# Kernel optimization log

Measured on AMD Instinct MI355X. Metric: run time of the kernel, lower is better.

Reference implementation:

```python
import jax, jax.numpy as jnp
import numpy as np

B, S, H, DH = 8, 2048, 16, 64
D = H * DH  # 1024; also the input feature dim
BIG_NEG = 1e8


def setup_inputs() -> dict:
    key = jax.random.key(0)
    ks = jax.random.split(key, 7)
    glorot = lambda k, shp: jax.random.normal(k, shp, jnp.float32) * np.sqrt(2.0 / (shp[0] + shp[1]))
    return {
        "Q_seq": jax.random.normal(ks[0], (B, S, D), jnp.float32),
        "K_seq": jax.random.normal(ks[1], (B, S, D), jnp.float32),
        "Q_mask": jnp.ones((B, S), jnp.float32),
        "K_mask": jnp.ones((B, S), jnp.float32),
        "WQ": glorot(ks[2], (D, D)),
        "WK": glorot(ks[3], (D, D)),
        "Wq": glorot(ks[4], (D, H)),
        "Wk": glorot(ks[5], (D, H)),
        "WP": glorot(ks[6], (D, D)),
    }


def reference(Q_seq, B_K_seq=None, **_unused):
    raise NotImplementedError  # placeholder overwritten below


def reference(Q_seq, K_seq, Q_mask, K_mask, WQ, WK, Wq, Wk, WP):
    scale = 1.0 / (DH ** 0.5)
    b, s, _ = Q_seq.shape

    Q = Q_seq @ WQ                                        # (B,S,D)
    # query additive attention over the sequence, per head
    q_logits = jnp.einsum('bsd,dh->bhs', Q, Wq) * scale   # (B,H,S)
    q_logits = q_logits - (1.0 - Q_mask[:, None, :]) * BIG_NEG
    q_att = jax.nn.softmax(q_logits, axis=-1)

    Qh = Q.reshape(b, s, H, DH).transpose(0, 2, 1, 3)     # (B,H,S,DH)
    Kh = (K_seq @ WK).reshape(b, s, H, DH).transpose(0, 2, 1, 3)

    global_q = jnp.einsum('bhs,bhsd->bhd', q_att, Qh)     # (B,H,DH)
    QK = Kh * global_q[:, :, None, :]                     # (B,H,S,DH)

    # NOTE: original reshapes (B,H,S,DH) straight to (B,S,H*DH) WITHOUT a
    # transpose (head-mixing raw reshape) — replicated faithfully here.
    QK_flat = QK.reshape(b, s, H * DH)
    k_logits = jnp.einsum('bsd,dh->bhs', QK_flat, Wk) * scale
    k_logits = k_logits - (1.0 - K_mask[:, None, :]) * BIG_NEG
    k_att = jax.nn.softmax(k_logits, axis=-1)

    global_k = jnp.einsum('bhs,bhsd->bhd', k_att, QK)     # (B,H,DH)
    QKQ = global_k[:, :, None, :] * Qh                    # (B,H,S,DH)

    out = QKQ.transpose(0, 2, 1, 3).reshape(b, s, H * DH) @ WP
    out = out.reshape(b, s, H, DH).transpose(0, 2, 1, 3) + Qh   # (B,H,S,DH)
    out = out.transpose(0, 2, 1, 3).reshape(b, s, H * DH)       # (B,S,D)
    return out
```

## Files before the change

### kernel.cpp

```cpp
#include <hip/hip_runtime.h>
#include <cstdint>
#include <cstddef>


#define B_ 8
#define S_ 2048
#define H_ 16
#define D_ 1024
#define SCALE_ 0.125f
#define BIGNEG_ 1e8f

typedef __attribute__((ext_vector_type(8))) __bf16 bf16x8;
typedef __attribute__((ext_vector_type(4))) float f32x4;

__device__ __forceinline__ unsigned short f2bf(float f) {
  unsigned int u = __float_as_uint(f);
  u += 0x7FFFu + ((u >> 16) & 1u);
  return (unsigned short)(u >> 16);
}
__device__ __forceinline__ float bf2f(unsigned short h) {
  return __uint_as_float(((unsigned int)h) << 16);
}

__device__ __forceinline__ void gll16(const void* g, void* l) {
  __builtin_amdgcn_global_load_lds(
      (__attribute__((address_space(1))) void*)(uintptr_t)g,
      (__attribute__((address_space(3))) void*)(uintptr_t)l,
      16, 0, 0);
}

__global__ __launch_bounds__(256) void k_conv(const float* __restrict__ in,
                                              unsigned short* __restrict__ out, int n4) {
  int i = blockIdx.x * 256 + threadIdx.x;
  if (i >= n4) return;
  float4 v = ((const float4*)in)[i];
  ushort4 o;
  o.x = f2bf(v.x); o.y = f2bf(v.y); o.z = f2bf(v.z); o.w = f2bf(v.w);
  ((ushort4*)out)[i] = o;
}

__global__ __launch_bounds__(256) void k_transpose3(
    const float* __restrict__ s0, unsigned short* __restrict__ d0,
    const float* __restrict__ s1, unsigned short* __restrict__ d1,
    const float* __restrict__ s2, unsigned short* __restrict__ d2,
    int K, int N) {
  const float* src = blockIdx.z == 0 ? s0 : (blockIdx.z == 1 ? s1 : s2);
  unsigned short* dst = blockIdx.z == 0 ? d0 : (blockIdx.z == 1 ? d1 : d2);
  __shared__ float tile[32][33];
  int n0 = blockIdx.x * 32, k0 = blockIdx.y * 32;
  int tx = threadIdx.x, ty = threadIdx.y;
#pragma unroll
  for (int i = 0; i < 4; i++) {
    int r = ty + i * 8;
    if (k0 + r < K && n0 + tx < N) tile[r][tx] = src[(size_t)(k0 + r) * N + n0 + tx];
  }
  __syncthreads();
#pragma unroll
  for (int i = 0; i < 4; i++) {
    int rn = ty + i * 8;
    if (n0 + rn < N && k0 + tx < K)
      dst[(size_t)(n0 + rn) * K + k0 + tx] = f2bf(tile[tx][rn]);
  }
}

__global__ __launch_bounds__(256) void k_transpose2(
    const float* __restrict__ s0, unsigned short* __restrict__ d0,
    const float* __restrict__ s1, unsigned short* __restrict__ d1,
    int K, int N) {
  const float* src = blockIdx.z == 0 ? s0 : s1;
  unsigned short* dst = blockIdx.z == 0 ? d0 : d1;
  __shared__ float tile[32][33];
  int n0 = blockIdx.x * 32, k0 = blockIdx.y * 32;
  int tx = threadIdx.x, ty = threadIdx.y;
#pragma unroll
  for (int i = 0; i < 4; i++) {
    int r = ty + i * 8;
    if (k0 + r < K && n0 + tx < N) tile[r][tx] = src[(size_t)(k0 + r) * N + n0 + tx];
  }
  __syncthreads();
#pragma unroll
  for (int i = 0; i < 4; i++) {
    int rn = ty + i * 8;
    if (n0 + rn < N && k0 + tx < K)
      dst[(size_t)(n0 + rn) * K + k0 + tx] = f2bf(tile[tx][rn]);
  }
}

__global__ __launch_bounds__(256) void k_gemm128(
    const unsigned short* __restrict__ A,
    const unsigned short* __restrict__ BTa, const unsigned short* __restrict__ BTb,
    int split, int bstride,
    unsigned short* __restrict__ Cbf, float* __restrict__ Cf,
    const unsigned short* __restrict__ Res,
    int M, int N, int K, int ntiles) {
  __shared__ unsigned short lA[128 * 64];
  __shared__ unsigned short lB[128 * 64];
  int t = threadIdx.x;
  int mt = blockIdx.x / ntiles, nt = blockIdx.x - mt * ntiles;
  int m0 = mt * 128, n0 = nt * 128;
  const unsigned short* BT =
      bstride ? (BTa + (size_t)(mt >> 4) * bstride) : (mt < split ? BTa : BTb);
  int lane = t & 63, w = t >> 6;
  int wm = (w >> 1) * 64, wn = (w & 1) * 64;
  int mq = lane & 15, q = lane >> 4;

  f32x4 zero = {0.f, 0.f, 0.f, 0.f};
  f32x4 acc[4][4];
#pragma unroll
  for (int i = 0; i < 4; i++)
#pragma unroll
    for (int j = 0; j < 4; j++) acc[i][j] = zero;

  const unsigned short* gA[4];
  const unsigned short* gB[4];
  unsigned short* pA[4];
  unsigned short* pB[4];
#pragma unroll
  for (int p = 0; p < 4; p++) {
    int g = t + p * 256;
    int row = g >> 3, c = g & 7;
    gA[p] = A + (size_t)(m0 + row) * K + c * 8;
    gB[p] = BT + (size_t)(n0 + row) * K + c * 8;
    pA[p] = &lA[g * 8];
    pB[p] = &lB[g * 8];
  }

  for (int k0 = 0; k0 < K; k0 += 64) {
#pragma unroll
    for (int p = 0; p < 4; p++) gll16(gA[p] + k0, pA[p]);
#pragma unroll
    for (int p = 0; p < 4; p++) gll16(gB[p] + k0, pB[p]);
    __syncthreads();
#pragma unroll
    for (int kk = 0; kk < 2; kk++) {
      bf16x8 av[4], bv[4];
#pragma unroll
      for (int i = 0; i < 4; i++)
        av[i] = *(const bf16x8*)&lA[(wm + i * 16 + mq) * 64 + kk * 32 + q * 8];
#pragma unroll
      for (int i = 0; i < 4; i++)
        bv[i] = *(const bf16x8*)&lB[(wn + i * 16 + mq) * 64 + kk * 32 + q * 8];
#pragma unroll
      for (int i = 0; i < 4; i++)
#pragma unroll
        for (int j = 0; j < 4; j++)
          acc[i][j] = __builtin_amdgcn_mfma_f32_16x16x32_bf16(av[i], bv[j], acc[i][j], 0, 0, 0);
    }
    __syncthreads();
  }

#pragma unroll
  for (int i = 0; i < 4; i++)
#pragma unroll
    for (int j = 0; j < 4; j++)
#pragma unroll
      for (int r = 0; r < 4; r++) {
        int row = m0 + wm + i * 16 + q * 4 + r;
        int col = n0 + wn + j * 16 + mq;
        size_t o = (size_t)row * N + col;
        float v = acc[i][j][r];
        if (Res) v += bf2f(Res[o]);
        if (Cf) Cf[o] = v;
        if (Cbf) Cbf[o] = f2bf(v);
      }
}

__global__ __launch_bounds__(256) void k_logits16(
    const unsigned short* __restrict__ A,
    const unsigned short* __restrict__ BT16,
    const float* __restrict__ mask,
    float* __restrict__ outl,
    int K) {
  __shared__ unsigned short lA[128 * 32];
  int t = threadIdx.x;
  int m0 = blockIdx.x * 128;
  int lane = t & 63, w = t >> 6;
  int mq = lane & 15, q = lane >> 4;
  f32x4 zero = {0.f, 0.f, 0.f, 0.f};
  f32x4 acc0 = zero, acc1 = zero;
  int f0 = t, f1 = t + 256;
  const unsigned short* gA0 = A + (size_t)(m0 + (f0 >> 2)) * K + (f0 & 3) * 8;
  const unsigned short* gA1 = A + (size_t)(m0 + (f1 >> 2)) * K + (f1 & 3) * 8;
  unsigned short* pA0 = &lA[f0 * 8];
  unsigned short* pA1 = &lA[f1 * 8];
  for (int k0 = 0; k0 < K; k0 += 32) {
    gll16(gA0 + k0, pA0);
    gll16(gA1 + k0, pA1);
    bf16x8 bv = *(const bf16x8*)&BT16[(size_t)mq * K + k0 + q * 8];
    __syncthreads();
    bf16x8 a0 = *(const bf16x8*)&lA[(w * 32 + mq) * 32 + q * 8];
    bf16x8 a1 = *(const bf16x8*)&lA[(w * 32 + 16 + mq) * 32 + q * 8];
    acc0 = __builtin_amdgcn_mfma_f32_16x16x32_bf16(a0, bv, acc0, 0, 0, 0);
    acc1 = __builtin_amdgcn_mfma_f32_16x16x32_bf16(a1, bv, acc1, 0, 0, 0);
    __syncthreads();
  }
#pragma unroll
  for (int im = 0; im < 2; im++)
#pragma unroll
    for (int r = 0; r < 4; r++) {
      int row = m0 + w * 32 + im * 16 + q * 4 + r;
      int b = row >> 11, s = row & 2047;
      float v = (im == 0 ? acc0[r] : acc1[r]) * SCALE_ - (1.0f - mask[row]) * BIGNEG_;
      outl[((size_t)(b * 16 + mq)) * 2048 + s] = v;
    }
}

__global__ __launch_bounds__(256) void k_logits16g(
    const unsigned short* __restrict__ Khbf,
    const unsigned short* __restrict__ WkT,
    const float* __restrict__ gq,
    const float* __restrict__ mask,
    float* __restrict__ outl) {
  __shared__ unsigned short lA[128 * 32];
  int t = threadIdx.x;
  int m0 = blockIdx.x * 128;
  int bb = m0 >> 11, h2 = (m0 >> 7) & 15;
  int lane = t & 63, w = t >> 6;
  int mq = lane & 15, q = lane >> 4;
  f32x4 zero = {0.f, 0.f, 0.f, 0.f};
  f32x4 acc0 = zero, acc1 = zero;
  int f0 = t, f1 = t + 256;
  int r0 = f0 >> 2, c0 = f0 & 3;
  int r1 = f1 >> 2, c1 = f1 & 3;
  const unsigned short* base = Khbf + (size_t)bb * 2048 * 1024 + h2 * 64;
  const float* gqb = gq + bb * 1024 + h2 * 64;
  unsigned short* pA0 = &lA[f0 * 8];
  unsigned short* pA1 = &lA[f1 * 8];
  for (int k0 = 0; k0 < 1024; k0 += 32) {
    int kc0 = k0 + c0 * 8, kc1 = k0 + c1 * 8;
    gll16(base + (size_t)(16 * r0 + (kc0 >> 6)) * 1024 + (kc0 & 63), pA0);
    gll16(base + (size_t)(16 * r1 + (kc1 >> 6)) * 1024 + (kc1 & 63), pA1);
    int kq = k0 + q * 8;
    bf16x8 wv = *(const bf16x8*)&WkT[(size_t)mq * 1024 + kq];
    float4 g0 = *(const float4*)&gqb[kq & 63];
    float4 g1 = *(const float4*)&gqb[(kq & 63) + 4];
    bf16x8 bv;
    bv[0] = (__bf16)((float)wv[0] * g0.x);
    bv[1] = (__bf16)((float)wv[1] * g0.y);
    bv[2] = (__bf16)((float)wv[2] * g0.z);
    bv[3] = (__bf16)((float)wv[3] * g0.w);
    bv[4] = (__bf16)((float)wv[4] * g1.x);
    bv[5] = (__bf16)((float)wv[5] * g1.y);
    bv[6] = (__bf16)((float)wv[6] * g1.z);
    bv[7] = (__bf16)((float)wv[7] * g1.w);
    __syncthreads();
    bf16x8 a0 = *(const bf16x8*)&lA[(w * 32 + mq) * 32 + q * 8];
    bf16x8 a1 = *(const bf16x8*)&lA[(w * 32 + 16 + mq) * 32 + q * 8];
    acc0 = __builtin_amdgcn_mfma_f32_16x16x32_bf16(a0, bv, acc0, 0, 0, 0);
    acc1 = __builtin_amdgcn_mfma_f32_16x16x32_bf16(a1, bv, acc1, 0, 0, 0);
    __syncthreads();
  }
#pragma unroll
  for (int im = 0; im < 2; im++)
#pragma unroll
    for (int r = 0; r < 4; r++) {
      int row = m0 + w * 32 + im * 16 + q * 4 + r;
      int b = row >> 11, s = row & 2047;
      float v = (im == 0 ? acc0[r] : acc1[r]) * SCALE_ - (1.0f - mask[row]) * BIGNEG_;
      outl[((size_t)(b * 16 + mq)) * 2048 + s] = v;
    }
}

__global__ __launch_bounds__(256) void k_softmax(float* __restrict__ logits) {
  __shared__ float red[8];
  int t = threadIdx.x;
  int lane = t & 63, w = t >> 6;
  float* lg = logits + (size_t)blockIdx.x * 2048;
  float4 a = ((const float4*)lg)[t];
  float4 b = ((const float4*)lg)[t + 256];
  float mx = fmaxf(fmaxf(fmaxf(a.x, a.y), fmaxf(a.z, a.w)),
                   fmaxf(fmaxf(b.x, b.y), fmaxf(b.z, b.w)));
#pragma unroll
  for (int off = 32; off > 0; off >>= 1) mx = fmaxf(mx, __shfl_down(mx, off, 64));
  if (lane == 0) red[w] = mx;
  __syncthreads();
  mx = fmaxf(fmaxf(red[0], red[1]), fmaxf(red[2], red[3]));
  float4 ea, eb;
  ea.x = expf(a.x - mx); ea.y = expf(a.y - mx); ea.z = expf(a.z - mx); ea.w = expf(a.w - mx);
  eb.x = expf(b.x - mx); eb.y = expf(b.y - mx); eb.z = expf(b.z - mx); eb.w = expf(b.w - mx);
  float ps = ea.x + ea.y + ea.z + ea.w + eb.x + eb.y + eb.z + eb.w;
#pragma unroll
  for (int off = 32; off > 0; off >>= 1) ps += __shfl_down(ps, off, 64);
  if (lane == 0) red[4 + w] = ps;
  __syncthreads();
  float inv = 1.0f / (red[4] + red[5] + red[6] + red[7]);
  ea.x *= inv; ea.y *= inv; ea.z *= inv; ea.w *= inv;
  eb.x *= inv; eb.y *= inv; eb.z *= inv; eb.w *= inv;
  ((float4*)lg)[t] = ea;
  ((float4*)lg)[t + 256] = eb;
}

__global__ __launch_bounds__(256) void k_poolpart(
    const float* __restrict__ att,
    const unsigned short* __restrict__ X,
    float* __restrict__ partial) {
  __shared__ float satt[32 * 16];
  int c = blockIdx.x, b = blockIdx.y;
  int t = threadIdx.x;
  for (int i = t; i < 512; i += 256) {
    int sl = i >> 4, h = i & 15;
    satt[i] = att[(((size_t)b * 16 + h) << 11) + c * 32 + sl];
  }
  __syncthreads();
  int h = t >> 4;
  const ushort4* xp = (const ushort4*)X + ((size_t)b * 2048 + c * 32) * 256 + t;
  float4 acc = {0.f, 0.f, 0.f, 0.f};
#pragma unroll 8
  for (int sl = 0; sl < 32; sl++) {
    float av = satt[sl * 16 + h];
    ushort4 xv = xp[sl * 256];
    acc.x += av * bf2f(xv.x);
    acc.y += av * bf2f(xv.y);
    acc.z += av * bf2f(xv.z);
    acc.w += av * bf2f(xv.w);
  }
  ((float4*)partial)[((size_t)b * 64 + c) * 256 + t] = acc;
}

__global__ __launch_bounds__(256) void k_poolfin(
    const float* __restrict__ partial,
    const float* __restrict__ gmul,
    float* __restrict__ outp) {
  int oi = blockIdx.x * 256 + threadIdx.x;
  int b = oi >> 10;
  const float* pp = partial + (size_t)b * 64 * 1024 + (oi & 1023);
  float s = 0.f;
#pragma unroll 8
  for (int c = 0; c < 64; c++) s += pp[(size_t)c * 1024];
  if (gmul) s *= gmul[oi];
  outp[oi] = s;
}

__global__ __launch_bounds__(256) void k_wpb(
    const unsigned short* __restrict__ WPT,
    const float* __restrict__ gk,
    unsigned short* __restrict__ WPb) {
  int i = blockIdx.x * 256 + threadIdx.x;
  int flat4 = i * 4;
  int b = flat4 >> 20;
  int rem = flat4 & 1048575;
  int k = rem & 1023;
  ushort4 wv = *(const ushort4*)&WPT[rem];
  float4 gv = *(const float4*)&gk[b * 1024 + k];
  ushort4 o;
  o.x = f2bf(bf2f(wv.x) * gv.x);
  o.y = f2bf(bf2f(wv.y) * gv.y);
  o.z = f2bf(bf2f(wv.z) * gv.z);
  o.w = f2bf(bf2f(wv.w) * gv.w);
  *(ushort4*)&WPb[flat4] = o;
}

extern "C" void kernel_launch(void* const* d_in, const int* in_sizes, int n_in,
                              void* d_out, int out_size, void* d_ws, size_t ws_size,
                              hipStream_t stream) {
  const float* Qseq  = (const float*)d_in[0];
  const float* Kseq  = (const float*)d_in[1];
  const float* Qmask = (const float*)d_in[2];
  const float* Kmask = (const float*)d_in[3];
  const float* WQ    = (const float*)d_in[4];
  const float* WK    = (const float*)d_in[5];
  const float* Wq    = (const float*)d_in[6];
  const float* Wk    = (const float*)d_in[7];
  const float* WP    = (const float*)d_in[8];
  float* out = (float*)d_out;

  const size_t SD = (size_t)B_ * S_ * D_;
  unsigned short* Qbf  = (unsigned short*)d_ws;
  unsigned short* Khbf = Qbf + SD;
  unsigned short* buf0 = Khbf + SD;
  unsigned short* WQT  = buf0 + SD;
  unsigned short* WKT  = WQT + (size_t)D_ * D_;
  unsigned short* WPT  = WKT + (size_t)D_ * D_;
  unsigned short* WqT  = WPT + (size_t)D_ * D_;
  unsigned short* WkT  = WqT + (size_t)H_ * D_;
  float* ql = (float*)(WkT + (size_t)H_ * D_);
  float* kl = ql + (size_t)B_ * H_ * S_;
  float* gq = kl + (size_t)B_ * H_ * S_;
  float* gk = gq + (size_t)B_ * D_;
  float* partial = (float*)buf0;
  unsigned short* WPb = buf0 + 2 * 1024 * 1024;

  dim3 blk256(256);
  dim3 tblk(32, 8);
  int n4 = (int)(SD / 4);
  dim3 convGrid((n4 + 255) / 256);
  const int M = B_ * S_;

  k_transpose3<<<dim3(32, 32, 3), tblk, 0, stream>>>(WQ, WQT, WK, WKT, WP, WPT, D_, D_);
  k_transpose2<<<dim3(1, 32, 2), tblk, 0, stream>>>(Wq, WqT, Wk, WkT, D_, H_);

  k_conv<<<convGrid, blk256, 0, stream>>>(Qseq, buf0, n4);
  k_gemm128<<<dim3(1024), blk256, 0, stream>>>(buf0, WQT, WQT, 1 << 30, 0,
                                               Qbf, (float*)nullptr,
                                               (const unsigned short*)nullptr, M, D_, D_, 8);
  k_conv<<<convGrid, blk256, 0, stream>>>(Kseq, buf0, n4);
  k_gemm128<<<dim3(1024), blk256, 0, stream>>>(buf0, WKT, WKT, 1 << 30, 0,
                                               Khbf, (float*)nullptr,
                                               (const unsigned short*)nullptr, M, D_, D_, 8);

  k_logits16<<<dim3(128), blk256, 0, stream>>>(Qbf, WqT, Qmask, ql, D_);
  k_softmax<<<dim3(128), blk256, 0, stream>>>(ql);
  k_poolpart<<<dim3(64, 8), blk256, 0, stream>>>(ql, Qbf, partial);
  k_poolfin<<<dim3(32), blk256, 0, stream>>>(partial, (const float*)nullptr, gq);

  k_logits16g<<<dim3(128), blk256, 0, stream>>>(Khbf, WkT, gq, Kmask, kl);
  k_softmax<<<dim3(128), blk256, 0, stream>>>(kl);
  k_poolpart<<<dim3(64, 8), blk256, 0, stream>>>(kl, Khbf, partial);
  k_poolfin<<<dim3(32), blk256, 0, stream>>>(partial, gq, gk);

  k_wpb<<<dim3(8192), blk256, 0, stream>>>(WPT, gk, WPb);
  k_gemm128<<<dim3(1024), blk256, 0, stream>>>(Qbf, WPb, WPb, 0, 1 << 20,
                                               (unsigned short*)nullptr, out, Qbf,
                                               M, D_, D_, 8);
}
```

Before: 457.6 us.

## Batch Q/K conversion and projection GEMMs into single launches; swizzle GEMM LDS

Merges the two fp32-to-bf16 conversion launches into one kernel and the two projection GEMMs (Q@WQ, K@WK) into one 2048-block launch, staging the converted K input in the output buffer. The GEMM tiles now use an XOR swizzle on the 16-byte column groups, applied on both the global-to-LDS load and the MFMA operand reads, to reduce LDS bank conflicts. This cuts launch count and gives the GPU a larger grid per launch, at the cost of reusing the output buffer as scratch.

```diff
diff --git a/kernel.cpp b/kernel.cpp
--- a/kernel.cpp
+++ b/kernel.cpp
@@ -29,10 +29,13 @@
       16, 0, 0);
 }
 
-__global__ __launch_bounds__(256) void k_conv(const float* __restrict__ in,
-                                              unsigned short* __restrict__ out, int n4) {
+__global__ __launch_bounds__(256) void k_conv2(
+    const float* __restrict__ in0, unsigned short* __restrict__ out0,
+    const float* __restrict__ in1, unsigned short* __restrict__ out1, int n4) {
   int i = blockIdx.x * 256 + threadIdx.x;
-  if (i >= n4) return;
+  const float* in = in0;
+  unsigned short* out = out0;
+  if (i >= n4) { i -= n4; in = in1; out = out1; }
   float4 v = ((const float4*)in)[i];
   ushort4 o;
   o.x = f2bf(v.x); o.y = f2bf(v.y); o.z = f2bf(v.z); o.w = f2bf(v.w);
@@ -87,19 +90,22 @@
 }
 
 __global__ __launch_bounds__(256) void k_gemm128(
-    const unsigned short* __restrict__ A,
+    const unsigned short* __restrict__ A, const unsigned short* __restrict__ Aalt,
+    int asplit,
     const unsigned short* __restrict__ BTa, const unsigned short* __restrict__ BTb,
-    int split, int bstride,
-    unsigned short* __restrict__ Cbf, float* __restrict__ Cf,
-    const unsigned short* __restrict__ Res,
-    int M, int N, int K, int ntiles) {
+    int bstride,
+    unsigned short* __restrict__ Cbf, unsigned short* __restrict__ Calt,
+    float* __restrict__ Cf, const unsigned short* __restrict__ Res,
+    int N, int K, int ntiles) {
   __shared__ unsigned short lA[128 * 64];
   __shared__ unsigned short lB[128 * 64];
   int t = threadIdx.x;
   int mt = blockIdx.x / ntiles, nt = blockIdx.x - mt * ntiles;
+  const unsigned short* BT = BTa;
+  unsigned short* Cb = Cbf;
+  if (mt >= asplit) { mt -= asplit; A = Aalt; BT = BTb; Cb = Calt; }
+  if (bstride) BT += (size_t)(mt >> 4) * bstride;
   int m0 = mt * 128, n0 = nt * 128;
-  const unsigned short* BT =
-      bstride ? (BTa + (size_t)(mt >> 4) * bstride) : (mt < split ? BTa : BTb);
   int lane = t & 63, w = t >> 6;
   int wm = (w >> 1) * 64, wn = (w & 1) * 64;
   int mq = lane & 15, q = lane >> 4;
@@ -118,13 +124,14 @@
 #pragma unroll
   for (int p = 0; p < 4; p++) {
     int g = t + p * 256;
-    int row = g >> 3, c = g & 7;
-    gA[p] = A + (size_t)(m0 + row) * K + c * 8;
-    gB[p] = BT + (size_t)(n0 + row) * K + c * 8;
+    int row = g >> 3, cg = (g & 7) ^ (row & 7);
+    gA[p] = A + (size_t)(m0 + row) * K + cg * 8;
+    gB[p] = BT + (size_t)(n0 + row) * K + cg * 8;
     pA[p] = &lA[g * 8];
     pB[p] = &lB[g * 8];
   }
 
+  int xa = mq & 7;
   for (int k0 = 0; k0 < K; k0 += 64) {
 #pragma unroll
     for (int p = 0; p < 4; p++) gll16(gA[p] + k0, pA[p]);
@@ -133,13 +140,14 @@
     __syncthreads();
 #pragma unroll
     for (int kk = 0; kk < 2; kk++) {
+      int xo = ((kk * 4 + q) ^ xa) * 8;
       bf16x8 av[4], bv[4];
 #pragma unroll
       for (int i = 0; i < 4; i++)
-        av[i] = *(const bf16x8*)&lA[(wm + i * 16 + mq) * 64 + kk * 32 + q * 8];
+        av[i] = *(const bf16x8*)&lA[(wm + i * 16 + mq) * 64 + xo];
 #pragma unroll
       for (int i = 0; i < 4; i++)
-        bv[i] = *(const bf16x8*)&lB[(wn + i * 16 + mq) * 64 + kk * 32 + q * 8];
+        bv[i] = *(const bf16x8*)&lB[(wn + i * 16 + mq) * 64 + xo];
 #pragma unroll
       for (int i = 0; i < 4; i++)
 #pragma unroll
@@ -161,7 +169,7 @@
         float v = acc[i][j][r];
         if (Res) v += bf2f(Res[o]);
         if (Cf) Cf[o] = v;
-        if (Cbf) Cbf[o] = f2bf(v);
+        if (Cb) Cb[o] = f2bf(v);
       }
 }
 
@@ -379,24 +387,21 @@
   float* gk = gq + (size_t)B_ * D_;
   float* partial = (float*)buf0;
   unsigned short* WPb = buf0 + 2 * 1024 * 1024;
+  unsigned short* Kstage = (unsigned short*)d_out;
 
   dim3 blk256(256);
   dim3 tblk(32, 8);
   int n4 = (int)(SD / 4);
-  dim3 convGrid((n4 + 255) / 256);
   const int M = B_ * S_;
 
   k_transpose3<<<dim3(32, 32, 3), tblk, 0, stream>>>(WQ, WQT, WK, WKT, WP, WPT, D_, D_);
   k_transpose2<<<dim3(1, 32, 2), tblk, 0, stream>>>(Wq, WqT, Wk, WkT, D_, H_);
 
-  k_conv<<<convGrid, blk256, 0, stream>>>(Qseq, buf0, n4);
-  k_gemm128<<<dim3(1024), blk256, 0, stream>>>(buf0, WQT, WQT, 1 << 30, 0,
-                                               Qbf, (float*)nullptr,
-                                               (const unsigned short*)nullptr, M, D_, D_, 8);
-  k_conv<<<convGrid, blk256, 0, stream>>>(Kseq, buf0, n4);
-  k_gemm128<<<dim3(1024), blk256, 0, stream>>>(buf0, WKT, WKT, 1 << 30, 0,
-                                               Khbf, (float*)nullptr,
-                                               (const unsigned short*)nullptr, M, D_, D_, 8);
+  k_conv2<<<dim3(2 * ((n4 + 255) / 256)), blk256, 0, stream>>>(Qseq, buf0, Kseq, Kstage, n4);
+
+  k_gemm128<<<dim3(2048), blk256, 0, stream>>>(buf0, Kstage, 128, WQT, WKT, 0,
+                                               Qbf, Khbf, (float*)nullptr,
+                                               (const unsigned short*)nullptr, D_, D_, 8);
 
   k_logits16<<<dim3(128), blk256, 0, stream>>>(Qbf, WqT, Qmask, ql, D_);
   k_softmax<<<dim3(128), blk256, 0, stream>>>(ql);
@@ -409,7 +414,7 @@
   k_poolfin<<<dim3(32), blk256, 0, stream>>>(partial, gq, gk);
 
   k_wpb<<<dim3(8192), blk256, 0, stream>>>(WPT, gk, WPb);
-  k_gemm128<<<dim3(1024), blk256, 0, stream>>>(Qbf, WPb, WPb, 0, 1 << 20,
-                                               (unsigned short*)nullptr, out, Qbf,
-                                               M, D_, D_, 8);
-}
+  k_gemm128<<<dim3(1024), blk256, 0, stream>>>(Qbf, Qbf, 1 << 30, WPb, WPb, 1 << 20,
+                                               (unsigned short*)nullptr, (unsigned short*)nullptr,
+                                               out, Qbf, D_, D_, 8);
+}
```

New measurement: 438.1 us. 1.04x faster.
